# Kernel optimization log

Hardware: AMD Instinct MI355X
Metric: run time of the kernel (lower is better)

Reference implementation:

```python
import jax, jax.numpy as jnp
import numpy as np

LN_EPS = 1e-5


def setup_inputs() -> dict:
    key = jax.random.key(0)
    B, S, D = 4, 4096, 1024
    x = jax.random.normal(key, (B, S, D), dtype=jnp.float32)
    gamma = jnp.ones((D,), dtype=jnp.float32)
    beta = jnp.zeros((D,), dtype=jnp.float32)
    return {"x": x, "gamma": gamma, "beta": beta}


def reference(x, gamma, beta):
    # LayerNorm over last dim (embed_dim), matching nn.LayerNorm(eps=1e-5)
    mean = jnp.mean(x, axis=-1, keepdims=True)
    var = jnp.mean(jnp.square(x - mean), axis=-1, keepdims=True)
    xn = (x - mean) / jnp.sqrt(var + LN_EPS)
    xn = xn * gamma + beta
    # FFT along hidden dim then along sequence dim; keep real part.
    f = jnp.fft.fft(jnp.fft.fft(xn, axis=-1), axis=-2)
    return jnp.real(f)
```

## Files before the change

kernel.cpp:

```cpp
#include <hip/hip_runtime.h>
#include <math.h>

#define LN_EPS 1e-5f

constexpr int D = 1024;
constexpr int S = 4096;
constexpr int B = 4;
constexpr int KH = 512;
constexpr float NEG_TWO_PI = -6.283185307179586f;
constexpr float RSQ2 = 0.70710678118654752f;

__device__ __forceinline__ float2 cmul(float2 a, float2 b) {
    return make_float2(a.x * b.x - a.y * b.y, a.x * b.y + a.y * b.x);
}
__device__ __forceinline__ float2 csq(float2 a) {
    return make_float2(a.x * a.x - a.y * a.y, 2.f * a.x * a.y);
}
__device__ __forceinline__ float2 cadd(float2 a, float2 b) { return make_float2(a.x + b.x, a.y + b.y); }
__device__ __forceinline__ float2 csub(float2 a, float2 b) { return make_float2(a.x - b.x, a.y - b.y); }
__device__ __forceinline__ float2 cnegi(float2 a) { return make_float2(a.y, -a.x); }
__device__ __forceinline__ float2 cposi(float2 a) { return make_float2(-a.y, a.x); }

__device__ __forceinline__ int P(int a) { return a + (a >> 4); }

__device__ __forceinline__ int rev4_10(int v) {
    unsigned br = __brev((unsigned)v) >> 22;
    return (int)(((br & 0x155u) << 1) | ((br & 0x2AAu) >> 1));
}

__device__ __forceinline__ void dft8(float2& c0, float2& c1, float2& c2, float2& c3,
                                     float2& c4, float2& c5, float2& c6, float2& c7) {
    float2 t0 = cadd(c0, c4), t1 = csub(c0, c4);
    float2 t2 = cadd(c2, c6), t3 = csub(c2, c6);
    float2 t4 = cadd(c1, c5), t5 = csub(c1, c5);
    float2 t6 = cadd(c3, c7), t7 = csub(c3, c7);
    float2 E0 = cadd(t0, t2), E2 = csub(t0, t2);
    float2 E1 = cadd(t1, cnegi(t3)), E3 = cadd(t1, cposi(t3));
    float2 O0 = cadd(t4, t6), O2 = csub(t4, t6);
    float2 O1 = cadd(t5, cnegi(t7)), O3 = cadd(t5, cposi(t7));
    float2 W1O1 = make_float2(RSQ2 * (O1.x + O1.y), RSQ2 * (O1.y - O1.x));
    float2 W2O2 = cnegi(O2);
    float2 W3O3 = make_float2(RSQ2 * (O3.y - O3.x), -RSQ2 * (O3.x + O3.y));
    c0 = cadd(E0, O0); c4 = csub(E0, O0);
    c1 = cadd(E1, W1O1); c5 = csub(E1, W1O1);
    c2 = cadd(E2, W2O2); c6 = csub(E2, W2O2);
    c3 = cadd(E3, W3O3); c7 = csub(E3, W3O3);
}

__device__ __forceinline__ void fft64_rows_512(float2* tile, const float2* tw64) {
    {
        int col = threadIdx.x & 63;
        int g = threadIdx.x >> 6;
#define R0(mm) tile[((((g) << 3) | (mm)) << 6) | col]
        float2 c0 = R0(0), c1 = R0(1), c2 = R0(2), c3 = R0(3);
        float2 c4 = R0(4), c5 = R0(5), c6 = R0(6), c7 = R0(7);
        dft8(c0, c1, c2, c3, c4, c5, c6, c7);
        R0(0) = c0; R0(1) = c1; R0(2) = c2; R0(3) = c3;
        R0(4) = c4; R0(5) = c5; R0(6) = c6; R0(7) = c7;
#undef R0
    }
    __syncthreads();
    {
        int col = threadIdx.x & 63;
        int j = threadIdx.x >> 6;
#define R1(mm) tile[(((j) + ((mm) << 3)) << 6) | col]
        float2 c0 = R1(0);
        float2 c1 = cmul(R1(1), tw64[j]);
        float2 c2 = cmul(R1(2), tw64[2 * j]);
        float2 c3 = cmul(R1(3), tw64[3 * j]);
        float2 c4 = cmul(R1(4), tw64[4 * j]);
        float2 c5 = cmul(R1(5), tw64[5 * j]);
        float2 c6 = cmul(R1(6), tw64[6 * j]);
        float2 c7 = cmul(R1(7), tw64[7 * j]);
        dft8(c0, c1, c2, c3, c4, c5, c6, c7);
        R1(0) = c0; R1(1) = c1; R1(2) = c2; R1(3) = c3;
        R1(4) = c4; R1(5) = c5; R1(6) = c6; R1(7) = c7;
#undef R1
    }
    __syncthreads();
}

__global__ __launch_bounds__(256) void ln_fft_d(const float* __restrict__ x,
                                                const float* __restrict__ gamma,
                                                const float* __restrict__ beta,
                                                float2* __restrict__ y) {
    __shared__ float2 cx[1088];
    __shared__ float2 twA[256];
    __shared__ float red[36];

    const int tid = threadIdx.x;
    const size_t row0 = (size_t)blockIdx.x * 2;
    const float* x0 = x + row0 * D;
    const float* x1 = x0 + D;

    float wsn, wcs;
    __sincosf(NEG_TWO_PI * (float)tid * (1.0f / 1024.0f), &wsn, &wcs);
    const float2 w1s0 = make_float2(wcs, wsn);
    twA[tid] = w1s0;

    float a0[4], a1[4];
    float s0 = 0.f, q0 = 0.f, s1 = 0.f, q1 = 0.f;
#pragma unroll
    for (int j = 0; j < 4; ++j) {
        float u = x0[tid + (j << 8)];
        float v = x1[tid + (j << 8)];
        a0[j] = u; a1[j] = v;
        s0 += u; q0 += u * u; s1 += v; q1 += v * v;
    }
#pragma unroll
    for (int off = 32; off; off >>= 1) {
        s0 += __shfl_down(s0, off); q0 += __shfl_down(q0, off);
        s1 += __shfl_down(s1, off); q1 += __shfl_down(q1, off);
    }
    const int wid = tid >> 6;
    if ((tid & 63) == 0) { red[wid] = s0; red[8 + wid] = q0; red[16 + wid] = s1; red[24 + wid] = q1; }
    __syncthreads();
    if (tid == 0) {
        float S0 = red[0] + red[1] + red[2] + red[3];
        float Q0 = red[8] + red[9] + red[10] + red[11];
        float S1 = red[16] + red[17] + red[18] + red[19];
        float Q1 = red[24] + red[25] + red[26] + red[27];
        float m0 = S0 * (1.0f / D), m1 = S1 * (1.0f / D);
        red[32] = m0; red[33] = rsqrtf(Q0 * (1.0f / D) - m0 * m0 + LN_EPS);
        red[34] = m1; red[35] = rsqrtf(Q1 * (1.0f / D) - m1 * m1 + LN_EPS);
    }
    __syncthreads();
    const float m0 = red[32], r0 = red[33], m1 = red[34], r1 = red[35];

    float2 A0, A1, A2, A3;
    {
        float gg, bb;
        gg = gamma[tid];       bb = beta[tid];
        A0 = make_float2((a0[0] - m0) * r0 * gg + bb, (a1[0] - m1) * r1 * gg + bb);
        gg = gamma[tid + 256]; bb = beta[tid + 256];
        A1 = make_float2((a0[1] - m0) * r0 * gg + bb, (a1[1] - m1) * r1 * gg + bb);
        gg = gamma[tid + 512]; bb = beta[tid + 512];
        A2 = make_float2((a0[2] - m0) * r0 * gg + bb, (a1[2] - m1) * r1 * gg + bb);
        gg = gamma[tid + 768]; bb = beta[tid + 768];
        A3 = make_float2((a0[3] - m0) * r0 * gg + bb, (a1[3] - m1) * r1 * gg + bb);
    }
    {
        float2 b0 = cadd(A0, A2), b1 = csub(A0, A2);
        float2 b2 = cadd(A1, A3), b3 = csub(A1, A3);
        float2 w2 = csq(w1s0), w3 = cmul(w1s0, w2);
        cx[P(tid)]       = cadd(b0, b2);
        cx[P(tid + 256)] = cmul(cadd(b1, cnegi(b3)), w1s0);
        cx[P(tid + 512)] = cmul(csub(b0, b2), w2);
        cx[P(tid + 768)] = cmul(cadd(b1, cposi(b3)), w3);
    }
    __syncthreads();

#pragma unroll
    for (int sIdx = 0; sIdx < 3; ++sIdx) {
        const int lL = 8 - 2 * sIdx;
        const int qq = 1 << (lL - 2);
        const int j = tid & (qq - 1);
        const int base = ((tid >> (lL - 2)) << lL) | j;
        const float2 w1 = twA[j << (10 - lL)];
        const float2 w2 = csq(w1), w3 = cmul(w1, w2);
        const int p0 = P(base), p1 = P(base + qq), p2 = P(base + 2 * qq), p3 = P(base + 3 * qq);
        float2 B0 = cx[p0], B1 = cx[p1], B2 = cx[p2], B3 = cx[p3];
        float2 b0 = cadd(B0, B2), b1 = csub(B0, B2);
        float2 b2 = cadd(B1, B3), b3 = csub(B1, B3);
        cx[p0] = cadd(b0, b2);
        cx[p1] = cmul(cadd(b1, cnegi(b3)), w1);
        cx[p2] = cmul(csub(b0, b2), w2);
        cx[p3] = cmul(cadd(b1, cposi(b3)), w3);
        __syncthreads();
    }
    {
        const int base = tid << 2;
        const int p0 = P(base), p1 = P(base + 1), p2 = P(base + 2), p3 = P(base + 3);
        float2 B0 = cx[p0], B1 = cx[p1], B2 = cx[p2], B3 = cx[p3];
        float2 b0 = cadd(B0, B2), b1 = csub(B0, B2);
        float2 b2 = cadd(B1, B3), b3 = csub(B1, B3);
        cx[p0] = cadd(b0, b2);
        cx[p1] = cadd(b1, cnegi(b3));
        cx[p2] = csub(b0, b2);
        cx[p3] = cadd(b1, cposi(b3));
    }
    __syncthreads();

    float2* y0 = y + row0 * KH;
    float2* y1 = y0 + KH;
    if (tid == 0) {
        float2 X0 = cx[P(0)];
        float2 X512 = cx[P(2)];
        y0[0] = make_float2(X0.x, X512.x);
        y1[0] = make_float2(X0.y, X512.y);
    } else {
        int kc = tid;
        float2 XA = cx[P(rev4_10(kc))];
        float2 XB = cx[P(rev4_10(1024 - kc))];
        y0[kc] = make_float2(0.5f * (XA.x + XB.x), 0.5f * (XA.y - XB.y));
        y1[kc] = make_float2(0.5f * (XA.y + XB.y), 0.5f * (XB.x - XA.x));
    }
    {
        int kc = tid + 256;
        float2 XA = cx[P(rev4_10(kc))];
        float2 XB = cx[P(rev4_10(1024 - kc))];
        y0[kc] = make_float2(0.5f * (XA.x + XB.x), 0.5f * (XA.y - XB.y));
        y1[kc] = make_float2(0.5f * (XA.y + XB.y), 0.5f * (XB.x - XA.x));
    }
}

__global__ __launch_bounds__(512, 8) void fft_s_p1(const float2* y, float2* z) {
    __shared__ float2 tile[64 * 64];
    __shared__ float2 tw64[64];

    const int bid = blockIdx.x;
    const int dt = bid & 7;
    const int n1 = (bid >> 3) & 63;
    const int b  = bid >> 9;
    const int d0 = dt << 6;
    const int t = threadIdx.x;
    const int l32 = t & 31;
    const int rgrp = t >> 5;

    if (t < 64) {
        float sn, c;
        __sincosf(NEG_TWO_PI * (float)t * (1.0f / 64.0f), &sn, &c);
        tw64[t] = make_float2(c, sn);
    }

#pragma unroll
    for (int m = 0; m < 4; ++m) {
        int n2 = (m << 4) | rgrp;
        int rr = ((n2 & 7) << 3) | (n2 >> 3);
        const float4* src = (const float4*)(y + (size_t)((b << 12) | (n2 << 6) | n1) * KH + d0);
        ((float4*)tile)[(rr << 5) | l32] = src[l32];
    }
    __syncthreads();

    fft64_rows_512(tile, tw64);

    float2 wq, wstep;
    {
        float sn, c;
        __sincosf(NEG_TWO_PI * (float)(n1 * rgrp) * (1.0f / 4096.0f), &sn, &c);
        wq = make_float2(c, sn);
        __sincosf(NEG_TWO_PI * (float)n1 * (1.0f / 256.0f), &sn, &c);
        wstep = make_float2(c, sn);
    }
#pragma unroll
    for (int m = 0; m < 4; ++m) {
        int k2 = (m << 4) | rgrp;
        float4 v4 = ((const float4*)tile)[(k2 << 5) | l32];
        float2 a = cmul(make_float2(v4.x, v4.y), wq);
        float2 c = cmul(make_float2(v4.z, v4.w), wq);
        float4* dst = (float4*)(z + (size_t)((b << 12) | (k2 << 6) | n1) * KH + d0);
        dst[l32] = make_float4(a.x, a.y, c.x, c.y);
        wq = cmul(wq, wstep);
    }
}

__global__ __launch_bounds__(512, 8) void fft_s_p2(const float2* __restrict__ z,
                                                   float* __restrict__ out) {
    __shared__ float2 tile[64 * 64];
    __shared__ float2 tw64[64];

    const int t = threadIdx.x;
    if (t < 64) {
        float sn, c;
        __sincosf(NEG_TWO_PI * (float)t * (1.0f / 64.0f), &sn, &c);
        tw64[t] = make_float2(c, sn);
    }

    if (blockIdx.x < B * 64 * 8) {
        const int bid = blockIdx.x;
        const int dt = bid & 7;
        const int k2 = (bid >> 3) & 63;
        const int b  = bid >> 9;
        const int d0 = dt << 6;
        const int l32 = t & 31;
        const int rgrp = t >> 5;

#pragma unroll
        for (int m = 0; m < 4; ++m) {
            int n1 = (m << 4) | rgrp;
            int rr = ((n1 & 7) << 3) | (n1 >> 3);
            const float4* src = (const float4*)(z + (size_t)((b << 12) | (k2 << 6) | n1) * KH + d0);
            ((float4*)tile)[(rr << 5) | l32] = src[l32];
        }
        __syncthreads();

        fft64_rows_512(tile, tw64);

        const int kc0 = d0 + (l32 << 1);
#pragma unroll
        for (int m = 0; m < 4; ++m) {
            int k1 = (m << 4) | rgrp;
            int q = (k1 << 6) | k2;
            float4 v4 = ((const float4*)tile)[(k1 << 5) | l32];
            size_t rowo = ((size_t)(b << 12) + (size_t)q) * D;
            int qm = (S - q) & (S - 1);
            size_t rowm = ((size_t)(b << 12) + (size_t)qm) * D;
            if (kc0) {
                *(float2*)(out + rowo + kc0) = make_float2(v4.x, v4.z);
                out[rowm + (D - kc0)]     = v4.x;
                out[rowm + (D - kc0 - 1)] = v4.z;
            } else {
                out[rowo + 1]       = v4.z;
                out[rowm + (D - 1)] = v4.z;
            }
        }
    } else {
        const int b = blockIdx.x - B * 64 * 8;
        const int lane = t & 63;
        const int r8   = t >> 6;

#pragma unroll
        for (int m = 0; m < 8; ++m) {
            int k2 = (m << 3) | r8;
            int rr = ((lane & 7) << 3) | (lane >> 3);
            tile[(rr << 6) | k2] = z[(size_t)((b << 12) | (k2 << 6) | lane) * KH];
        }
        __syncthreads();

        fft64_rows_512(tile, tw64);

#pragma unroll
        for (int m = 0; m < 8; ++m) {
            int k1 = (m << 3) | r8;
            int k2 = lane;
            int q = (k1 << 6) | k2;
            int k2m = (64 - k2) & 63;
            int k1m = (k2 == 0) ? ((64 - k1) & 63) : (63 - k1);
            float2 Hq = tile[(k1 << 6) | k2];
            float2 Hm = tile[(k1m << 6) | k2m];
            size_t ob = ((size_t)(b << 12) + (size_t)q) * D;
            out[ob]       = 0.5f * (Hq.x + Hm.x);
            out[ob + 512] = 0.5f * (Hq.y + Hm.y);
        }
    }
}

extern "C" void kernel_launch(void* const* d_in, const int* in_sizes, int n_in,
                              void* d_out, int out_size, void* d_ws, size_t ws_size,
                              hipStream_t stream) {
    const float* x     = (const float*)d_in[0];
    const float* gamma = (const float*)d_in[1];
    const float* beta  = (const float*)d_in[2];
    float* out = (float*)d_out;

    float2* y = (float2*)d_ws;

    ln_fft_d<<<B * S / 2, 256, 0, stream>>>(x, gamma, beta, y);
    fft_s_p1<<<B * 64 * 8, 512, 0, stream>>>(y, y);
    fft_s_p2<<<B * 64 * 8 + B, 512, 0, stream>>>(y, out);
}
```

Baseline: 180.7 us.

## Narrow sequence-FFT tiles to 32 columns, split DC column kernel, repad LDS

The sequence-axis FFT kernels now process 64x32 tiles with 256 threads instead of 64x64 tiles with 512 threads, doubling the block count and halving shared memory per block. The special DC/Nyquist column work moves out of fft_s_p2 into a separate small kernel, fft_s_c0, so the main kernel loses its divergent branch. The hidden-dim FFT switches to a padding function with an extra skew every 256 elements to cut shared-memory bank conflicts. The cost is an extra kernel launch and a 4-block tail kernel that runs serially after p2, and fft_s_p1 still updates y in place.

```diff
diff --git a/kernel.cpp b/kernel.cpp
--- a/kernel.cpp
+++ b/kernel.cpp
@@ -21,7 +21,7 @@
 __device__ __forceinline__ float2 cnegi(float2 a) { return make_float2(a.y, -a.x); }
 __device__ __forceinline__ float2 cposi(float2 a) { return make_float2(-a.y, a.x); }
 
-__device__ __forceinline__ int P(int a) { return a + (a >> 4); }
+__device__ __forceinline__ int P2(int a) { return a + (a >> 4) + (a >> 8); }
 
 __device__ __forceinline__ int rev4_10(int v) {
     unsigned br = __brev((unsigned)v) >> 22;
@@ -47,10 +47,45 @@
     c3 = cadd(E3, W3O3); c7 = csub(E3, W3O3);
 }
 
-__device__ __forceinline__ void fft64_rows_512(float2* tile, const float2* tw64) {
-    {
-        int col = threadIdx.x & 63;
-        int g = threadIdx.x >> 6;
+__device__ __forceinline__ void fft64_rows_w32(float2* tile, const float2* tw64) {
+    {
+        int col = threadIdx.x & 31;
+        int g = threadIdx.x >> 5;
+#define R0(mm) tile[((((g) << 3) | (mm)) << 5) | col]
+        float2 c0 = R0(0), c1 = R0(1), c2 = R0(2), c3 = R0(3);
+        float2 c4 = R0(4), c5 = R0(5), c6 = R0(6), c7 = R0(7);
+        dft8(c0, c1, c2, c3, c4, c5, c6, c7);
+        R0(0) = c0; R0(1) = c1; R0(2) = c2; R0(3) = c3;
+        R0(4) = c4; R0(5) = c5; R0(6) = c6; R0(7) = c7;
+#undef R0
+    }
+    __syncthreads();
+    {
+        int col = threadIdx.x & 31;
+        int j = threadIdx.x >> 5;
+#define R1(mm) tile[(((j) + ((mm) << 3)) << 5) | col]
+        float2 c0 = R1(0);
+        float2 c1 = cmul(R1(1), tw64[j]);
+        float2 c2 = cmul(R1(2), tw64[2 * j]);
+        float2 c3 = cmul(R1(3), tw64[3 * j]);
+        float2 c4 = cmul(R1(4), tw64[4 * j]);
+        float2 c5 = cmul(R1(5), tw64[5 * j]);
+        float2 c6 = cmul(R1(6), tw64[6 * j]);
+        float2 c7 = cmul(R1(7), tw64[7 * j]);
+        dft8(c0, c1, c2, c3, c4, c5, c6, c7);
+        R1(0) = c0; R1(1) = c1; R1(2) = c2; R1(3) = c3;
+        R1(4) = c4; R1(5) = c5; R1(6) = c6; R1(7) = c7;
+#undef R1
+    }
+    __syncthreads();
+}
+
+__device__ __forceinline__ void fft64_rows_w64(float2* tile, const float2* tw64) {
+#pragma unroll
+    for (int h = 0; h < 2; ++h) {
+        int bf = threadIdx.x + (h << 8);
+        int col = bf & 63;
+        int g = bf >> 6;
 #define R0(mm) tile[((((g) << 3) | (mm)) << 6) | col]
         float2 c0 = R0(0), c1 = R0(1), c2 = R0(2), c3 = R0(3);
         float2 c4 = R0(4), c5 = R0(5), c6 = R0(6), c7 = R0(7);
@@ -60,9 +95,11 @@
 #undef R0
     }
     __syncthreads();
-    {
-        int col = threadIdx.x & 63;
-        int j = threadIdx.x >> 6;
+#pragma unroll
+    for (int h = 0; h < 2; ++h) {
+        int bf = threadIdx.x + (h << 8);
+        int col = bf & 63;
+        int j = bf >> 6;
 #define R1(mm) tile[(((j) + ((mm) << 3)) << 6) | col]
         float2 c0 = R1(0);
         float2 c1 = cmul(R1(1), tw64[j]);
@@ -84,7 +121,7 @@
                                                 const float* __restrict__ gamma,
                                                 const float* __restrict__ beta,
                                                 float2* __restrict__ y) {
-    __shared__ float2 cx[1088];
+    __shared__ float2 cx[1100];
     __shared__ float2 twA[256];
     __shared__ float red[36];
 
@@ -143,10 +180,10 @@
         float2 b0 = cadd(A0, A2), b1 = csub(A0, A2);
         float2 b2 = cadd(A1, A3), b3 = csub(A1, A3);
         float2 w2 = csq(w1s0), w3 = cmul(w1s0, w2);
-        cx[P(tid)]       = cadd(b0, b2);
-        cx[P(tid + 256)] = cmul(cadd(b1, cnegi(b3)), w1s0);
-        cx[P(tid + 512)] = cmul(csub(b0, b2), w2);
-        cx[P(tid + 768)] = cmul(cadd(b1, cposi(b3)), w3);
+        cx[P2(tid)]       = cadd(b0, b2);
+        cx[P2(tid + 256)] = cmul(cadd(b1, cnegi(b3)), w1s0);
+        cx[P2(tid + 512)] = cmul(csub(b0, b2), w2);
+        cx[P2(tid + 768)] = cmul(cadd(b1, cposi(b3)), w3);
     }
     __syncthreads();
 
@@ -158,7 +195,7 @@
         const int base = ((tid >> (lL - 2)) << lL) | j;
         const float2 w1 = twA[j << (10 - lL)];
         const float2 w2 = csq(w1), w3 = cmul(w1, w2);
-        const int p0 = P(base), p1 = P(base + qq), p2 = P(base + 2 * qq), p3 = P(base + 3 * qq);
+        const int p0 = P2(base), p1 = P2(base + qq), p2 = P2(base + 2 * qq), p3 = P2(base + 3 * qq);
         float2 B0 = cx[p0], B1 = cx[p1], B2 = cx[p2], B3 = cx[p3];
         float2 b0 = cadd(B0, B2), b1 = csub(B0, B2);
         float2 b2 = cadd(B1, B3), b3 = csub(B1, B3);
@@ -170,7 +207,7 @@
     }
     {
         const int base = tid << 2;
-        const int p0 = P(base), p1 = P(base + 1), p2 = P(base + 2), p3 = P(base + 3);
+        const int p0 = P2(base), p1 = P2(base + 1), p2 = P2(base + 2), p3 = P2(base + 3);
         float2 B0 = cx[p0], B1 = cx[p1], B2 = cx[p2], B3 = cx[p3];
         float2 b0 = cadd(B0, B2), b1 = csub(B0, B2);
         float2 b2 = cadd(B1, B3), b3 = csub(B1, B3);
@@ -184,38 +221,38 @@
     float2* y0 = y + row0 * KH;
     float2* y1 = y0 + KH;
     if (tid == 0) {
-        float2 X0 = cx[P(0)];
-        float2 X512 = cx[P(2)];
+        float2 X0 = cx[P2(0)];
+        float2 X512 = cx[P2(2)];
         y0[0] = make_float2(X0.x, X512.x);
         y1[0] = make_float2(X0.y, X512.y);
     } else {
         int kc = tid;
-        float2 XA = cx[P(rev4_10(kc))];
-        float2 XB = cx[P(rev4_10(1024 - kc))];
+        float2 XA = cx[P2(rev4_10(kc))];
+        float2 XB = cx[P2(rev4_10(1024 - kc))];
         y0[kc] = make_float2(0.5f * (XA.x + XB.x), 0.5f * (XA.y - XB.y));
         y1[kc] = make_float2(0.5f * (XA.y + XB.y), 0.5f * (XB.x - XA.x));
     }
     {
         int kc = tid + 256;
-        float2 XA = cx[P(rev4_10(kc))];
-        float2 XB = cx[P(rev4_10(1024 - kc))];
+        float2 XA = cx[P2(rev4_10(kc))];
+        float2 XB = cx[P2(rev4_10(1024 - kc))];
         y0[kc] = make_float2(0.5f * (XA.x + XB.x), 0.5f * (XA.y - XB.y));
         y1[kc] = make_float2(0.5f * (XA.y + XB.y), 0.5f * (XB.x - XA.x));
     }
 }
 
-__global__ __launch_bounds__(512, 8) void fft_s_p1(const float2* y, float2* z) {
-    __shared__ float2 tile[64 * 64];
+__global__ __launch_bounds__(256) void fft_s_p1(const float2* y, float2* z) {
+    __shared__ float2 tile[64 * 32];
     __shared__ float2 tw64[64];
 
     const int bid = blockIdx.x;
-    const int dt = bid & 7;
-    const int n1 = (bid >> 3) & 63;
-    const int b  = bid >> 9;
-    const int d0 = dt << 6;
+    const int dt = bid & 15;
+    const int n1 = (bid >> 4) & 63;
+    const int b  = bid >> 10;
+    const int d0 = dt << 5;
     const int t = threadIdx.x;
-    const int l32 = t & 31;
-    const int rgrp = t >> 5;
+    const int l16 = t & 15;
+    const int rg  = t >> 4;
 
     if (t < 64) {
         float sn, c;
@@ -225,113 +262,124 @@
 
 #pragma unroll
     for (int m = 0; m < 4; ++m) {
-        int n2 = (m << 4) | rgrp;
+        int n2 = (m << 4) | rg;
         int rr = ((n2 & 7) << 3) | (n2 >> 3);
         const float4* src = (const float4*)(y + (size_t)((b << 12) | (n2 << 6) | n1) * KH + d0);
-        ((float4*)tile)[(rr << 5) | l32] = src[l32];
-    }
-    __syncthreads();
-
-    fft64_rows_512(tile, tw64);
+        ((float4*)tile)[(rr << 4) | l16] = src[l16];
+    }
+    __syncthreads();
+
+    fft64_rows_w32(tile, tw64);
 
     float2 wq, wstep;
     {
         float sn, c;
-        __sincosf(NEG_TWO_PI * (float)(n1 * rgrp) * (1.0f / 4096.0f), &sn, &c);
+        __sincosf(NEG_TWO_PI * (float)(n1 * rg) * (1.0f / 4096.0f), &sn, &c);
         wq = make_float2(c, sn);
         __sincosf(NEG_TWO_PI * (float)n1 * (1.0f / 256.0f), &sn, &c);
         wstep = make_float2(c, sn);
     }
 #pragma unroll
     for (int m = 0; m < 4; ++m) {
-        int k2 = (m << 4) | rgrp;
-        float4 v4 = ((const float4*)tile)[(k2 << 5) | l32];
+        int k2 = (m << 4) | rg;
+        float4 v4 = ((const float4*)tile)[(k2 << 4) | l16];
         float2 a = cmul(make_float2(v4.x, v4.y), wq);
         float2 c = cmul(make_float2(v4.z, v4.w), wq);
         float4* dst = (float4*)(z + (size_t)((b << 12) | (k2 << 6) | n1) * KH + d0);
-        dst[l32] = make_float4(a.x, a.y, c.x, c.y);
+        dst[l16] = make_float4(a.x, a.y, c.x, c.y);
         wq = cmul(wq, wstep);
     }
 }
 
-__global__ __launch_bounds__(512, 8) void fft_s_p2(const float2* __restrict__ z,
-                                                   float* __restrict__ out) {
-    __shared__ float2 tile[64 * 64];
+__global__ __launch_bounds__(256) void fft_s_p2(const float2* __restrict__ z,
+                                                float* __restrict__ out) {
+    __shared__ float2 tile[64 * 32];
     __shared__ float2 tw64[64];
 
+    const int bid = blockIdx.x;
+    const int dt = bid & 15;
+    const int k2 = (bid >> 4) & 63;
+    const int b  = bid >> 10;
+    const int d0 = dt << 5;
     const int t = threadIdx.x;
+    const int l16 = t & 15;
+    const int rg  = t >> 4;
+
     if (t < 64) {
         float sn, c;
         __sincosf(NEG_TWO_PI * (float)t * (1.0f / 64.0f), &sn, &c);
         tw64[t] = make_float2(c, sn);
     }
 
-    if (blockIdx.x < B * 64 * 8) {
-        const int bid = blockIdx.x;
-        const int dt = bid & 7;
-        const int k2 = (bid >> 3) & 63;
-        const int b  = bid >> 9;
-        const int d0 = dt << 6;
-        const int l32 = t & 31;
-        const int rgrp = t >> 5;
-
-#pragma unroll
-        for (int m = 0; m < 4; ++m) {
-            int n1 = (m << 4) | rgrp;
-            int rr = ((n1 & 7) << 3) | (n1 >> 3);
-            const float4* src = (const float4*)(z + (size_t)((b << 12) | (k2 << 6) | n1) * KH + d0);
-            ((float4*)tile)[(rr << 5) | l32] = src[l32];
+#pragma unroll
+    for (int m = 0; m < 4; ++m) {
+        int n1 = (m << 4) | rg;
+        int rr = ((n1 & 7) << 3) | (n1 >> 3);
+        const float4* src = (const float4*)(z + (size_t)((b << 12) | (k2 << 6) | n1) * KH + d0);
+        ((float4*)tile)[(rr << 4) | l16] = src[l16];
+    }
+    __syncthreads();
+
+    fft64_rows_w32(tile, tw64);
+
+    const int kc0 = d0 + (l16 << 1);
+#pragma unroll
+    for (int m = 0; m < 4; ++m) {
+        int k1 = (m << 4) | rg;
+        int q = (k1 << 6) | k2;
+        float4 v4 = ((const float4*)tile)[(k1 << 4) | l16];
+        size_t rowo = ((size_t)(b << 12) + (size_t)q) * D;
+        int qm = (S - q) & (S - 1);
+        size_t rowm = ((size_t)(b << 12) + (size_t)qm) * D;
+        if (kc0) {
+            *(float2*)(out + rowo + kc0) = make_float2(v4.x, v4.z);
+            out[rowm + (D - kc0)]     = v4.x;
+            out[rowm + (D - kc0 - 1)] = v4.z;
+        } else {
+            out[rowo + 1]       = v4.z;
+            out[rowm + (D - 1)] = v4.z;
         }
-        __syncthreads();
-
-        fft64_rows_512(tile, tw64);
-
-        const int kc0 = d0 + (l32 << 1);
-#pragma unroll
-        for (int m = 0; m < 4; ++m) {
-            int k1 = (m << 4) | rgrp;
-            int q = (k1 << 6) | k2;
-            float4 v4 = ((const float4*)tile)[(k1 << 5) | l32];
-            size_t rowo = ((size_t)(b << 12) + (size_t)q) * D;
-            int qm = (S - q) & (S - 1);
-            size_t rowm = ((size_t)(b << 12) + (size_t)qm) * D;
-            if (kc0) {
-                *(float2*)(out + rowo + kc0) = make_float2(v4.x, v4.z);
-                out[rowm + (D - kc0)]     = v4.x;
-                out[rowm + (D - kc0 - 1)] = v4.z;
-            } else {
-                out[rowo + 1]       = v4.z;
-                out[rowm + (D - 1)] = v4.z;
-            }
-        }
-    } else {
-        const int b = blockIdx.x - B * 64 * 8;
-        const int lane = t & 63;
-        const int r8   = t >> 6;
-
-#pragma unroll
-        for (int m = 0; m < 8; ++m) {
-            int k2 = (m << 3) | r8;
-            int rr = ((lane & 7) << 3) | (lane >> 3);
-            tile[(rr << 6) | k2] = z[(size_t)((b << 12) | (k2 << 6) | lane) * KH];
-        }
-        __syncthreads();
-
-        fft64_rows_512(tile, tw64);
-
-#pragma unroll
-        for (int m = 0; m < 8; ++m) {
-            int k1 = (m << 3) | r8;
-            int k2 = lane;
-            int q = (k1 << 6) | k2;
-            int k2m = (64 - k2) & 63;
-            int k1m = (k2 == 0) ? ((64 - k1) & 63) : (63 - k1);
-            float2 Hq = tile[(k1 << 6) | k2];
-            float2 Hm = tile[(k1m << 6) | k2m];
-            size_t ob = ((size_t)(b << 12) + (size_t)q) * D;
-            out[ob]       = 0.5f * (Hq.x + Hm.x);
-            out[ob + 512] = 0.5f * (Hq.y + Hm.y);
-        }
+    }
+}
+
+__global__ __launch_bounds__(256) void fft_s_c0(const float2* __restrict__ z,
+                                                float* __restrict__ out) {
+    __shared__ float2 tile[64 * 64];
+    __shared__ float2 tw64[64];
+
+    const int b = blockIdx.x;
+    const int t = threadIdx.x;
+    const int lane = t & 63;
+    const int r4   = t >> 6;
+
+    if (t < 64) {
+        float sn, c;
+        __sincosf(NEG_TWO_PI * (float)t * (1.0f / 64.0f), &sn, &c);
+        tw64[t] = make_float2(c, sn);
+    }
+
+#pragma unroll
+    for (int m = 0; m < 16; ++m) {
+        int k2 = (m << 2) | r4;
+        int rr = ((lane & 7) << 3) | (lane >> 3);
+        tile[(rr << 6) | k2] = z[(size_t)((b << 12) | (k2 << 6) | lane) * KH];
+    }
+    __syncthreads();
+
+    fft64_rows_w64(tile, tw64);
+
+#pragma unroll
+    for (int m = 0; m < 16; ++m) {
+        int k1 = (m << 2) | r4;
+        int k2 = lane;
+        int q = (k1 << 6) | k2;
+        int k2m = (64 - k2) & 63;
+        int k1m = (k2 == 0) ? ((64 - k1) & 63) : (63 - k1);
+        float2 Hq = tile[(k1 << 6) | k2];
+        float2 Hm = tile[(k1m << 6) | k2m];
+        size_t ob = ((size_t)(b << 12) + (size_t)q) * D;
+        out[ob]       = 0.5f * (Hq.x + Hm.x);
+        out[ob + 512] = 0.5f * (Hq.y + Hm.y);
     }
 }
 
@@ -346,6 +394,7 @@
     float2* y = (float2*)d_ws;
 
     ln_fft_d<<<B * S / 2, 256, 0, stream>>>(x, gamma, beta, y);
-    fft_s_p1<<<B * 64 * 8, 512, 0, stream>>>(y, y);
-    fft_s_p2<<<B * 64 * 8 + B, 512, 0, stream>>>(y, out);
-}
+    fft_s_p1<<<B * 64 * 16, 256, 0, stream>>>(y, y);
+    fft_s_p2<<<B * 64 * 16, 256, 0, stream>>>(y, out);
+    fft_s_c0<<<B, 256, 0, stream>>>(y, out);
+}
```

New measurement: 187.1 us. +3.5%, slower.
